# Performance work log

Hardware: AMD Instinct MI355X
Metric: run time of the kernel (lower is better)

The kernel has to match this reference:

```python
import jax, jax.numpy as jnp
import numpy as np

DIM = 1024
H = 16
D = DIM // H  # head_dim = 64
SCALE = 1.0 / (D ** 0.5 * 1.0)  # 1/(sqrt(head_dim)*temperature)
MIN_CUTOFF = 1e-15


def setup_inputs() -> dict:
    key = jax.random.key(0)
    ks = jax.random.split(key, 6)
    B, T = 2, 2048
    x = jax.random.normal(ks[0], (B, T, DIM), dtype=jnp.float32)
    cutoffs = jax.random.uniform(ks[1], (B, T, T), dtype=jnp.float32)
    # torch nn.Linear params: weight [out, in], bias [out]
    W_qkv = jax.random.normal(ks[2], (3 * DIM, DIM), dtype=jnp.float32) * (DIM ** -0.5)
    b_qkv = jax.random.normal(ks[3], (3 * DIM,), dtype=jnp.float32) * 0.01
    W_out = jax.random.normal(ks[4], (DIM, DIM), dtype=jnp.float32) * (DIM ** -0.5)
    b_out = jax.random.normal(ks[5], (DIM,), dtype=jnp.float32) * 0.01
    return {"x": x, "cutoffs": cutoffs, "W_qkv": W_qkv, "b_qkv": b_qkv,
            "W_out": W_out, "b_out": b_out}


def reference(x, cutoffs, W_qkv, b_qkv, W_out, b_out):
    B, T, _ = x.shape
    # QKV projection -> [B, T, 3, H, D] -> [3, B, H, T, D]
    qkv = (jnp.einsum('btc,oc->bto', x, W_qkv) + b_qkv)
    qkv = qkv.reshape(B, T, 3, H, D).transpose(2, 0, 3, 1, 4)
    q, k, v = qkv[0], qkv[1], qkv[2]
    # additive log-bias from cutoffs, broadcast over heads
    bias = jnp.log(jnp.clip(cutoffs, MIN_CUTOFF, None))[:, None, :, :]  # [B,1,T,T]
    scores = jnp.einsum('bhqd,bhkd->bhqk', q, k) * SCALE + bias
    attn = jax.nn.softmax(scores, axis=-1)
    out = jnp.einsum('bhqk,bhkd->bhqd', attn, v)  # [B,H,T,D]
    out = out.transpose(0, 2, 1, 3).reshape(B, T, DIM)
    return jnp.einsum('btc,oc->bto', out, W_out) + b_out
```

## Files before the change

kernel.cpp:

```cpp
#include <hip/hip_runtime.h>

typedef __attribute__((ext_vector_type(4))) float f32x4;
typedef __attribute__((ext_vector_type(8))) short bf16x8;

__device__ __forceinline__ unsigned short f2bf(float f) {
    union { float f; unsigned u; } v; v.f = f;
    unsigned r = v.u + 0x7FFFu + ((v.u >> 16) & 1u);
    return (unsigned short)(r >> 16);
}

#define GLD16(gp, lp)                                                          \
    __builtin_amdgcn_global_load_lds(                                          \
        (const __attribute__((address_space(1))) void*)(gp),                   \
        (__attribute__((address_space(3))) void*)(lp), 16, 0, 0)

__global__ void k_cvt(const float* __restrict__ in, unsigned short* __restrict__ out, int n4) {
    int i = blockIdx.x * blockDim.x + threadIdx.x;
    int stride = gridDim.x * blockDim.x;
    for (; i < n4; i += stride) {
        float4 v = reinterpret_cast<const float4*>(in)[i];
        ushort4 o;
        o.x = f2bf(v.x); o.y = f2bf(v.y); o.z = f2bf(v.z); o.w = f2bf(v.w);
        reinterpret_cast<ushort4*>(out)[i] = o;
    }
}

__global__ void k_log(const float* __restrict__ in, float* __restrict__ out, int n4) {
    int i = blockIdx.x * blockDim.x + threadIdx.x;
    int stride = gridDim.x * blockDim.x;
    for (; i < n4; i += stride) {
        float4 v = reinterpret_cast<const float4*>(in)[i];
        float4 o;
        o.x = __logf(fmaxf(v.x, 1e-15f));
        o.y = __logf(fmaxf(v.y, 1e-15f));
        o.z = __logf(fmaxf(v.z, 1e-15f));
        o.w = __logf(fmaxf(v.w, 1e-15f));
        reinterpret_cast<float4*>(out)[i] = o;
    }
}

template <int MODE>
__global__ __launch_bounds__(256) void gemm_bt(
    const unsigned short* __restrict__ A, const unsigned short* __restrict__ B,
    const float* __restrict__ bias, float* __restrict__ outf,
    unsigned short* __restrict__ qb, unsigned short* __restrict__ kb,
    unsigned short* __restrict__ vb, int M, int N, int K)
{
    __shared__ unsigned short sA[128 * 32];
    __shared__ unsigned short sB[128 * 32];
    const int tid = threadIdx.x;
    const int w = tid >> 6, lane = tid & 63, g = lane >> 4, r = lane & 15;
    const int tm = blockIdx.x * 128, tn = blockIdx.y * 128;
    const int wr = w >> 1, wc = w & 1;

    f32x4 acc[4][4];
#pragma unroll
    for (int i = 0; i < 4; i++)
#pragma unroll
        for (int j = 0; j < 4; j++) acc[i][j] = (f32x4)0.f;

    const unsigned short* ga0 = A + (size_t)(tm + w * 32 + (lane >> 2)) * K + (lane & 3) * 8;
    const unsigned short* gb0 = B + (size_t)(tn + w * 32 + (lane >> 2)) * K + (lane & 3) * 8;
    unsigned short* la = sA + w * 32 * 32;
    unsigned short* lb = sB + w * 32 * 32;

    for (int kk = 0; kk < K; kk += 32) {
        __syncthreads();
        GLD16(ga0 + kk, la);
        GLD16(ga0 + kk + (size_t)16 * K, la + 16 * 32);
        GLD16(gb0 + kk, lb);
        GLD16(gb0 + kk + (size_t)16 * K, lb + 16 * 32);
        __syncthreads();
        bf16x8 af[4], bfv[4];
#pragma unroll
        for (int f = 0; f < 4; f++) af[f] = *(const bf16x8*)&sA[(wr * 64 + f * 16 + r) * 32 + g * 8];
#pragma unroll
        for (int f = 0; f < 4; f++) bfv[f] = *(const bf16x8*)&sB[(wc * 64 + f * 16 + r) * 32 + g * 8];
#pragma unroll
        for (int i = 0; i < 4; i++)
#pragma unroll
            for (int j = 0; j < 4; j++)
                acc[i][j] = __builtin_amdgcn_mfma_f32_16x16x32_bf16(af[i], bfv[j], acc[i][j], 0, 0, 0);
    }

#pragma unroll
    for (int fj = 0; fj < 4; fj++) {
        int n = tn + wc * 64 + fj * 16 + r;
        float bn = bias[n];
#pragma unroll
        for (int fi = 0; fi < 4; fi++) {
#pragma unroll
            for (int j = 0; j < 4; j++) {
                int m = tm + wr * 64 + fi * 16 + 4 * g + j;
                float v = acc[fi][fj][j] + bn;
                if (MODE == 0) {
                    outf[(size_t)m * N + n] = v;
                } else {
                    int three = n >> 10, h = (n >> 6) & 15, d = n & 63;
                    int b = m >> 11, t = m & 2047, bh = b * 16 + h;
                    unsigned short bv = f2bf(v);
                    if (three == 0)      qb[((size_t)bh * 2048 + t) * 64 + d] = bv;
                    else if (three == 1) kb[((size_t)bh * 2048 + t) * 64 + d] = bv;
                    else                 vb[((size_t)bh * 64 + d) * 2048 + t] = bv;
                }
            }
        }
    }
}

__global__ __launch_bounds__(256) void attn_kernel(
    const unsigned short* __restrict__ qbuf, const unsigned short* __restrict__ kbuf,
    const unsigned short* __restrict__ vbuf, const float* __restrict__ logbias,
    unsigned short* __restrict__ outa)
{
    __shared__ unsigned short sQ[64 * 64], sK[64 * 64], sV[64 * 64], sP[4 * 16 * 64];
    const int tid = threadIdx.x, w = tid >> 6, lane = tid & 63, g = lane >> 4, r = lane & 15;
    const int qt = blockIdx.x, h = blockIdx.y, b = blockIdx.z;
    const int q0 = qt * 64, bh = b * 16 + h;

    {
        int c = lane & 7;
#pragma unroll
        for (int i = 0; i < 2; i++) {
            int row = w * 16 + i * 8 + (lane >> 3);
            GLD16(qbuf + ((size_t)bh * 2048 + q0 + row) * 64 + (c ^ (row & 7)) * 8,
                  sQ + (w * 16 + i * 8) * 64);
        }
    }
    __syncthreads();
    bf16x8 aq[2];
    {
        int qrow = w * 16 + r;
#pragma unroll
        for (int s = 0; s < 2; s++)
            aq[s] = *(const bf16x8*)&sQ[qrow * 64 + ((s * 32 + g * 8) ^ ((qrow & 7) << 3))];
    }

    f32x4 oacc[4];
#pragma unroll
    for (int f = 0; f < 4; f++) oacc[f] = (f32x4)0.f;
    float mrow[4], lrow[4];
#pragma unroll
    for (int j = 0; j < 4; j++) { mrow[j] = -1e30f; lrow[j] = 0.f; }

    unsigned short* sPw = sP + w * 16 * 64;

    for (int kt = 0; kt < 32; kt++) {
        __syncthreads();
        {
            int c = lane & 7;
#pragma unroll
            for (int i = 0; i < 2; i++) {
                int row = w * 16 + i * 8 + (lane >> 3);
                GLD16(kbuf + ((size_t)bh * 2048 + kt * 64 + row) * 64 + (c ^ (row & 7)) * 8,
                      sK + (w * 16 + i * 8) * 64);
                GLD16(vbuf + ((size_t)bh * 64 + row) * 2048 + kt * 64 + (c ^ (row & 7)) * 8,
                      sV + (w * 16 + i * 8) * 64);
            }
        }
        float bias[4][4];
#pragma unroll
        for (int f = 0; f < 4; f++)
#pragma unroll
            for (int j = 0; j < 4; j++)
                bias[f][j] = logbias[((size_t)b * 2048 + (q0 + w * 16 + 4 * g + j)) * 2048
                                     + kt * 64 + f * 16 + r];
        __syncthreads();

        f32x4 sa[4];
#pragma unroll
        for (int f = 0; f < 4; f++) sa[f] = (f32x4)0.f;
#pragma unroll
        for (int s = 0; s < 2; s++)
#pragma unroll
            for (int f = 0; f < 4; f++) {
                int krow = f * 16 + r;
                bf16x8 bk = *(const bf16x8*)&sK[krow * 64 + ((s * 32 + g * 8) ^ ((krow & 7) << 3))];
                sa[f] = __builtin_amdgcn_mfma_f32_16x16x32_bf16(aq[s], bk, sa[f], 0, 0, 0);
            }

        float sv[4][4];
#pragma unroll
        for (int f = 0; f < 4; f++)
#pragma unroll
            for (int j = 0; j < 4; j++) sv[f][j] = sa[f][j] * 0.125f + bias[f][j];

        float alpha[4], psum[4];
#pragma unroll
        for (int j = 0; j < 4; j++) {
            float pm = fmaxf(fmaxf(sv[0][j], sv[1][j]), fmaxf(sv[2][j], sv[3][j]));
            pm = fmaxf(pm, __shfl_xor(pm, 1));
            pm = fmaxf(pm, __shfl_xor(pm, 2));
            pm = fmaxf(pm, __shfl_xor(pm, 4));
            pm = fmaxf(pm, __shfl_xor(pm, 8));
            float mnew = fmaxf(mrow[j], pm);
            alpha[j] = __expf(mrow[j] - mnew);
            mrow[j] = mnew;
            psum[j] = 0.f;
        }
#pragma unroll
        for (int f = 0; f < 4; f++)
#pragma unroll
            for (int j = 0; j < 4; j++) {
                float p = __expf(sv[f][j] - mrow[j]);
                psum[j] += p;
                int row = 4 * g + j, col = f * 16 + r;
                sPw[row * 64 + (col ^ ((row & 7) << 3))] = f2bf(p);
            }
#pragma unroll
        for (int j = 0; j < 4; j++) {
            psum[j] += __shfl_xor(psum[j], 1);
            psum[j] += __shfl_xor(psum[j], 2);
            psum[j] += __shfl_xor(psum[j], 4);
            psum[j] += __shfl_xor(psum[j], 8);
            lrow[j] = lrow[j] * alpha[j] + psum[j];
            oacc[0][j] *= alpha[j]; oacc[1][j] *= alpha[j];
            oacc[2][j] *= alpha[j]; oacc[3][j] *= alpha[j];
        }

#pragma unroll
        for (int s = 0; s < 2; s++) {
            bf16x8 pa = *(const bf16x8*)&sPw[r * 64 + ((s * 32 + g * 8) ^ ((r & 7) << 3))];
#pragma unroll
            for (int f = 0; f < 4; f++) {
                int drow = f * 16 + r;
                bf16x8 bvv = *(const bf16x8*)&sV[drow * 64 + ((s * 32 + g * 8) ^ ((drow & 7) << 3))];
                oacc[f] = __builtin_amdgcn_mfma_f32_16x16x32_bf16(pa, bvv, oacc[f], 0, 0, 0);
            }
        }
    }

#pragma unroll
    for (int j = 0; j < 4; j++) {
        float inv = 1.f / lrow[j];
        int q = q0 + w * 16 + 4 * g + j;
#pragma unroll
        for (int f = 0; f < 4; f++) {
            int d = f * 16 + r;
            outa[((size_t)(b * 2048 + q)) * 1024 + h * 64 + d] = f2bf(oacc[f][j] * inv);
        }
    }
}

extern "C" void kernel_launch(void* const* d_in, const int* in_sizes, int n_in,
                              void* d_out, int out_size, void* d_ws, size_t ws_size,
                              hipStream_t stream) {
    const float* x       = (const float*)d_in[0];
    const float* cutoffs = (const float*)d_in[1];
    const float* Wqkv    = (const float*)d_in[2];
    const float* bqkv    = (const float*)d_in[3];
    const float* Wout    = (const float*)d_in[4];
    const float* bout    = (const float*)d_in[5];
    float* out = (float*)d_out;

    char* ws = (char*)d_ws;
    float* logbias = (float*)ws;                    ws += (size_t)2 * 2048 * 2048 * 4;
    unsigned short* x_bf    = (unsigned short*)ws;  ws += (size_t)4096 * 1024 * 2;
    unsigned short* wqkv_bf = (unsigned short*)ws;  ws += (size_t)3072 * 1024 * 2;
    unsigned short* wout_bf = (unsigned short*)ws;  ws += (size_t)1024 * 1024 * 2;
    unsigned short* qb      = (unsigned short*)ws;  ws += (size_t)32 * 2048 * 64 * 2;
    unsigned short* kb      = (unsigned short*)ws;  ws += (size_t)32 * 2048 * 64 * 2;
    unsigned short* vb      = (unsigned short*)ws;  ws += (size_t)32 * 2048 * 64 * 2;
    unsigned short* attn_o  = (unsigned short*)ws;  ws += (size_t)4096 * 1024 * 2;

    k_cvt<<<1024, 256, 0, stream>>>(x,    x_bf,    4096 * 1024 / 4);
    k_cvt<<<1024, 256, 0, stream>>>(Wqkv, wqkv_bf, 3072 * 1024 / 4);
    k_cvt<<<512,  256, 0, stream>>>(Wout, wout_bf, 1024 * 1024 / 4);
    k_log<<<2048, 256, 0, stream>>>(cutoffs, logbias, 2 * 2048 * 2048 / 4);

    gemm_bt<1><<<dim3(32, 24), 256, 0, stream>>>(x_bf, wqkv_bf, bqkv, nullptr,
                                                 qb, kb, vb, 4096, 3072, 1024);
    attn_kernel<<<dim3(32, 16, 2), 256, 0, stream>>>(qb, kb, vb, logbias, attn_o);
    gemm_bt<0><<<dim3(32, 8), 256, 0, stream>>>(attn_o, wout_bf, bout, out,
                                                nullptr, nullptr, nullptr, 4096, 1024, 1024);
}
```

Measured before the change: 313.3 us.

## Fold log-bias into softmax as multiplicative cutoff; double-buffer GEMM and attention tiles

Drops the separate log kernel and its workspace buffer. The attention kernel now reads cutoffs directly and uses exp(s+log c)=c*exp(s), multiplying each probability by the clamped cutoff instead of adding a log bias. Both the GEMM and attention kernels double-buffer their LDS tiles, issuing the next tile's async loads before computing the current one, and Q is loaded straight to registers. The running max now ignores the bias, which could change numerical behaviour when cutoffs are tiny, and LDS use per block grows.

```diff
diff --git a/kernel.cpp b/kernel.cpp
--- a/kernel.cpp
+++ b/kernel.cpp
@@ -25,20 +25,6 @@
     }
 }
 
-__global__ void k_log(const float* __restrict__ in, float* __restrict__ out, int n4) {
-    int i = blockIdx.x * blockDim.x + threadIdx.x;
-    int stride = gridDim.x * blockDim.x;
-    for (; i < n4; i += stride) {
-        float4 v = reinterpret_cast<const float4*>(in)[i];
-        float4 o;
-        o.x = __logf(fmaxf(v.x, 1e-15f));
-        o.y = __logf(fmaxf(v.y, 1e-15f));
-        o.z = __logf(fmaxf(v.z, 1e-15f));
-        o.w = __logf(fmaxf(v.w, 1e-15f));
-        reinterpret_cast<float4*>(out)[i] = o;
-    }
-}
-
 template <int MODE>
 __global__ __launch_bounds__(256) void gemm_bt(
     const unsigned short* __restrict__ A, const unsigned short* __restrict__ B,
@@ -46,8 +32,8 @@
     unsigned short* __restrict__ qb, unsigned short* __restrict__ kb,
     unsigned short* __restrict__ vb, int M, int N, int K)
 {
-    __shared__ unsigned short sA[128 * 32];
-    __shared__ unsigned short sB[128 * 32];
+    __shared__ unsigned short sA[2][128 * 32];
+    __shared__ unsigned short sB[2][128 * 32];
     const int tid = threadIdx.x;
     const int w = tid >> 6, lane = tid & 63, g = lane >> 4, r = lane & 15;
     const int tm = blockIdx.x * 128, tn = blockIdx.y * 128;
@@ -61,26 +47,33 @@
 
     const unsigned short* ga0 = A + (size_t)(tm + w * 32 + (lane >> 2)) * K + (lane & 3) * 8;
     const unsigned short* gb0 = B + (size_t)(tn + w * 32 + (lane >> 2)) * K + (lane & 3) * 8;
-    unsigned short* la = sA + w * 32 * 32;
-    unsigned short* lb = sB + w * 32 * 32;
-
+    const int lbase = w * 32 * 32;
+
+    auto stageAB = [&](int nb, int kk) {
+        GLD16(ga0 + kk, &sA[nb][lbase]);
+        GLD16(ga0 + kk + (size_t)16 * K, &sA[nb][lbase + 16 * 32]);
+        GLD16(gb0 + kk, &sB[nb][lbase]);
+        GLD16(gb0 + kk + (size_t)16 * K, &sB[nb][lbase + 16 * 32]);
+    };
+
+    stageAB(0, 0);
+    __syncthreads();
+
+#pragma unroll 2
     for (int kk = 0; kk < K; kk += 32) {
-        __syncthreads();
-        GLD16(ga0 + kk, la);
-        GLD16(ga0 + kk + (size_t)16 * K, la + 16 * 32);
-        GLD16(gb0 + kk, lb);
-        GLD16(gb0 + kk + (size_t)16 * K, lb + 16 * 32);
-        __syncthreads();
+        const int cur = (kk >> 5) & 1;
+        if (kk + 32 < K) stageAB(cur ^ 1, kk + 32);
         bf16x8 af[4], bfv[4];
 #pragma unroll
-        for (int f = 0; f < 4; f++) af[f] = *(const bf16x8*)&sA[(wr * 64 + f * 16 + r) * 32 + g * 8];
-#pragma unroll
-        for (int f = 0; f < 4; f++) bfv[f] = *(const bf16x8*)&sB[(wc * 64 + f * 16 + r) * 32 + g * 8];
+        for (int f = 0; f < 4; f++) af[f] = *(const bf16x8*)&sA[cur][(wr * 64 + f * 16 + r) * 32 + g * 8];
+#pragma unroll
+        for (int f = 0; f < 4; f++) bfv[f] = *(const bf16x8*)&sB[cur][(wc * 64 + f * 16 + r) * 32 + g * 8];
 #pragma unroll
         for (int i = 0; i < 4; i++)
 #pragma unroll
             for (int j = 0; j < 4; j++)
                 acc[i][j] = __builtin_amdgcn_mfma_f32_16x16x32_bf16(af[i], bfv[j], acc[i][j], 0, 0, 0);
+        __syncthreads();
     }
 
 #pragma unroll
@@ -110,31 +103,37 @@
 
 __global__ __launch_bounds__(256) void attn_kernel(
     const unsigned short* __restrict__ qbuf, const unsigned short* __restrict__ kbuf,
-    const unsigned short* __restrict__ vbuf, const float* __restrict__ logbias,
+    const unsigned short* __restrict__ vbuf, const float* __restrict__ cutoffs,
     unsigned short* __restrict__ outa)
 {
-    __shared__ unsigned short sQ[64 * 64], sK[64 * 64], sV[64 * 64], sP[4 * 16 * 64];
+    __shared__ unsigned short sK[2][64 * 64], sV[2][64 * 64], sP[4 * 16 * 64];
     const int tid = threadIdx.x, w = tid >> 6, lane = tid & 63, g = lane >> 4, r = lane & 15;
     const int qt = blockIdx.x, h = blockIdx.y, b = blockIdx.z;
     const int q0 = qt * 64, bh = b * 16 + h;
 
-    {
-        int c = lane & 7;
-#pragma unroll
-        for (int i = 0; i < 2; i++) {
-            int row = w * 16 + i * 8 + (lane >> 3);
-            GLD16(qbuf + ((size_t)bh * 2048 + q0 + row) * 64 + (c ^ (row & 7)) * 8,
-                  sQ + (w * 16 + i * 8) * 64);
-        }
-    }
-    __syncthreads();
     bf16x8 aq[2];
     {
-        int qrow = w * 16 + r;
-#pragma unroll
-        for (int s = 0; s < 2; s++)
-            aq[s] = *(const bf16x8*)&sQ[qrow * 64 + ((s * 32 + g * 8) ^ ((qrow & 7) << 3))];
-    }
+        const unsigned short* qp = qbuf + ((size_t)bh * 2048 + q0 + w * 16 + r) * 64;
+        aq[0] = *(const bf16x8*)(qp + g * 8);
+        aq[1] = *(const bf16x8*)(qp + 32 + g * 8);
+    }
+
+    const int c = lane & 7, rr = lane >> 3;
+    auto stage = [&](int nb, int kt) {
+#pragma unroll
+        for (int i = 0; i < 2; i++) {
+            int row = w * 16 + i * 8 + rr;
+            GLD16(kbuf + ((size_t)bh * 2048 + kt * 64 + row) * 64 + (c ^ (row & 7)) * 8,
+                  &sK[nb][(w * 16 + i * 8) * 64]);
+            GLD16(vbuf + ((size_t)bh * 64 + row) * 2048 + kt * 64 + (c ^ (row & 7)) * 8,
+                  &sV[nb][(w * 16 + i * 8) * 64]);
+        }
+    };
+
+    const float* cp[4];
+#pragma unroll
+    for (int j = 0; j < 4; j++)
+        cp[j] = cutoffs + ((size_t)b * 2048 + (q0 + w * 16 + 4 * g + j)) * 2048 + r;
 
     f32x4 oacc[4];
 #pragma unroll
@@ -145,27 +144,20 @@
 
     unsigned short* sPw = sP + w * 16 * 64;
 
+    stage(0, 0);
+    __syncthreads();
+
+#pragma unroll 2
     for (int kt = 0; kt < 32; kt++) {
-        __syncthreads();
-        {
-            int c = lane & 7;
-#pragma unroll
-            for (int i = 0; i < 2; i++) {
-                int row = w * 16 + i * 8 + (lane >> 3);
-                GLD16(kbuf + ((size_t)bh * 2048 + kt * 64 + row) * 64 + (c ^ (row & 7)) * 8,
-                      sK + (w * 16 + i * 8) * 64);
-                GLD16(vbuf + ((size_t)bh * 64 + row) * 2048 + kt * 64 + (c ^ (row & 7)) * 8,
-                      sV + (w * 16 + i * 8) * 64);
-            }
-        }
-        float bias[4][4];
+        const int cur = kt & 1;
+        if (kt < 31) stage(cur ^ 1, kt + 1);
+
+        float cut[4][4];
 #pragma unroll
         for (int f = 0; f < 4; f++)
 #pragma unroll
             for (int j = 0; j < 4; j++)
-                bias[f][j] = logbias[((size_t)b * 2048 + (q0 + w * 16 + 4 * g + j)) * 2048
-                                     + kt * 64 + f * 16 + r];
-        __syncthreads();
+                cut[f][j] = fmaxf(cp[j][kt * 64 + f * 16], 1e-15f);
 
         f32x4 sa[4];
 #pragma unroll
@@ -175,7 +167,7 @@
 #pragma unroll
             for (int f = 0; f < 4; f++) {
                 int krow = f * 16 + r;
-                bf16x8 bk = *(const bf16x8*)&sK[krow * 64 + ((s * 32 + g * 8) ^ ((krow & 7) << 3))];
+                bf16x8 bk = *(const bf16x8*)&sK[cur][krow * 64 + ((s * 32 + g * 8) ^ ((krow & 7) << 3))];
                 sa[f] = __builtin_amdgcn_mfma_f32_16x16x32_bf16(aq[s], bk, sa[f], 0, 0, 0);
             }
 
@@ -183,7 +175,7 @@
 #pragma unroll
         for (int f = 0; f < 4; f++)
 #pragma unroll
-            for (int j = 0; j < 4; j++) sv[f][j] = sa[f][j] * 0.125f + bias[f][j];
+            for (int j = 0; j < 4; j++) sv[f][j] = sa[f][j] * 0.125f;
 
         float alpha[4], psum[4];
 #pragma unroll
@@ -202,7 +194,7 @@
         for (int f = 0; f < 4; f++)
 #pragma unroll
             for (int j = 0; j < 4; j++) {
-                float p = __expf(sv[f][j] - mrow[j]);
+                float p = cut[f][j] * __expf(sv[f][j] - mrow[j]);
                 psum[j] += p;
                 int row = 4 * g + j, col = f * 16 + r;
                 sPw[row * 64 + (col ^ ((row & 7) << 3))] = f2bf(p);
@@ -224,10 +216,11 @@
 #pragma unroll
             for (int f = 0; f < 4; f++) {
                 int drow = f * 16 + r;
-                bf16x8 bvv = *(const bf16x8*)&sV[drow * 64 + ((s * 32 + g * 8) ^ ((drow & 7) << 3))];
+                bf16x8 bvv = *(const bf16x8*)&sV[cur][drow * 64 + ((s * 32 + g * 8) ^ ((drow & 7) << 3))];
                 oacc[f] = __builtin_amdgcn_mfma_f32_16x16x32_bf16(pa, bvv, oacc[f], 0, 0, 0);
             }
         }
+        __syncthreads();
     }
 
 #pragma unroll
@@ -254,7 +247,6 @@
     float* out = (float*)d_out;
 
     char* ws = (char*)d_ws;
-    float* logbias = (float*)ws;                    ws += (size_t)2 * 2048 * 2048 * 4;
     unsigned short* x_bf    = (unsigned short*)ws;  ws += (size_t)4096 * 1024 * 2;
     unsigned short* wqkv_bf = (unsigned short*)ws;  ws += (size_t)3072 * 1024 * 2;
     unsigned short* wout_bf = (unsigned short*)ws;  ws += (size_t)1024 * 1024 * 2;
@@ -266,11 +258,10 @@
     k_cvt<<<1024, 256, 0, stream>>>(x,    x_bf,    4096 * 1024 / 4);
     k_cvt<<<1024, 256, 0, stream>>>(Wqkv, wqkv_bf, 3072 * 1024 / 4);
     k_cvt<<<512,  256, 0, stream>>>(Wout, wout_bf, 1024 * 1024 / 4);
-    k_log<<<2048, 256, 0, stream>>>(cutoffs, logbias, 2 * 2048 * 2048 / 4);
 
     gemm_bt<1><<<dim3(32, 24), 256, 0, stream>>>(x_bf, wqkv_bf, bqkv, nullptr,
                                                  qb, kb, vb, 4096, 3072, 1024);
-    attn_kernel<<<dim3(32, 16, 2), 256, 0, stream>>>(qb, kb, vb, logbias, attn_o);
+    attn_kernel<<<dim3(32, 16, 2), 256, 0, stream>>>(qb, kb, vb, cutoffs, attn_o);
     gemm_bt<0><<<dim3(32, 8), 256, 0, stream>>>(attn_o, wout_bf, bout, out,
                                                 nullptr, nullptr, nullptr, 4096, 1024, 1024);
 }
```

After: 322.7 us. 1.03x slower.
